# Kernel tuning notes

Hardware: AMD Instinct MI355X
Metric: run time of the kernel (lower is better)

The kernel has to match this reference:

```python
import jax, jax.numpy as jnp
import numpy as np

L, D, H, B, SX, SY, VS, VT = 6, 1024, 16, 4, 512, 512, 32000, 32000
DK = D // H
FF = 4 * D
EPS = 1e-3          # LayerNorm eps (added to std, not var)
SCALE_EMB = float(np.sqrt(D))
NEG = -1e30         # stands in for -inf; fully-masked rows are zeroed after softmax


def pos_encoding(length, d):
    # tensor2tensor-style sinusoid: [sin | cos] concatenated along channels
    nt = d // 2
    lti = np.log(1e4) / (nt - 1)
    inv = np.exp(np.arange(nt) * -lti)
    st = np.arange(length)[:, None] * inv[None, :]
    return jnp.asarray(np.concatenate([np.sin(st), np.cos(st)], axis=1), jnp.float32)


def layer_norm(z, a, b):
    # faithful to the torch module: uses unbiased std (ddof=1) and divides by (std + eps)
    mu = z.mean(-1, keepdims=True)
    sig = jnp.sqrt(((z - mu) ** 2).sum(-1, keepdims=True) / (z.shape[-1] - 1))
    return (z - mu) / (sig + EPS) * a + b


def mha(xq, xkv, wq, wk, wv, wo, mask):
    # xq: (b, lq, D), xkv: (b, lk, D); head-chunking of channel dim == reshape to (H, DK)
    b, lq, _ = xq.shape
    q = (xq @ wq.T).reshape(b, lq, H, DK)
    k = (xkv @ wk.T).reshape(b, -1, H, DK)
    v = (xkv @ wv.T).reshape(b, -1, H, DK)
    s = jnp.einsum('bqhd,bkhd->bhqk', q, k) * (1.0 / np.sqrt(DK))
    m = mask[:, None, :, :]
    s = jnp.where(m, s, NEG)
    att = jax.nn.softmax(s, axis=-1)
    att = att * m.any(-1, keepdims=True)  # replicates NaN->0 for fully masked rows
    c = jnp.einsum('bhqk,bkhd->bqhd', att, v).reshape(b, lq, D)
    return c @ wo.T


def setup_inputs():
    key = jax.random.key(0)
    ks = jax.random.split(key, 10)
    s = 0.02
    emb_x = (jax.random.normal(ks[0], (VS, D), jnp.float32) * s).at[0].set(0.0)  # padding_idx=0
    emb_y = (jax.random.normal(ks[1], (VT, D), jnp.float32) * s).at[0].set(0.0)
    return {
        'emb_x': emb_x, 'emb_y': emb_y,
        'enc_qkvo': jax.random.normal(ks[2], (L, 4, D, D), jnp.float32) * s,
        'enc_ln_s': jnp.ones((L, 2, D), jnp.float32), 'enc_ln_b': jnp.zeros((L, 2, D), jnp.float32),
        'enc_w1': jax.random.normal(ks[3], (L, FF, D), jnp.float32) * s, 'enc_b1': jnp.zeros((L, FF), jnp.float32),
        'enc_w2': jax.random.normal(ks[4], (L, D, FF), jnp.float32) * s, 'enc_b2': jnp.zeros((L, D), jnp.float32),
        'dec_qkvo': jax.random.normal(ks[5], (L, 8, D, D), jnp.float32) * s,
        'dec_ln_s': jnp.ones((L, 3, D), jnp.float32), 'dec_ln_b': jnp.zeros((L, 3, D), jnp.float32),
        'dec_w1': jax.random.normal(ks[6], (L, FF, D), jnp.float32) * s, 'dec_b1': jnp.zeros((L, FF), jnp.float32),
        'dec_w2': jax.random.normal(ks[7], (L, D, FF), jnp.float32) * s, 'dec_b2': jnp.zeros((L, D), jnp.float32),
        'x_block': jax.random.randint(ks[8], (B, SX), 0, VS),
        'y_block': jax.random.randint(ks[9], (B, SY), 0, VT),
    }


def reference(emb_x, emb_y, enc_qkvo, enc_ln_s, enc_ln_b, enc_w1, enc_b1, enc_w2, enc_b2,
              dec_qkvo, dec_ln_s, dec_ln_b, dec_w1, dec_b1, dec_w2, dec_b2, x_block, y_block):
    # internal layout (b, len, D); torch code uses (b, D, len) -- math is identical
    ex = emb_x[x_block] * SCALE_EMB + pos_encoding(SX, D)[None]
    ey = emb_y[y_block] * SCALE_EMB + pos_encoding(SY, D)[None]
    xv = x_block != 0
    yv = y_block != 0
    xx = xv[:, :, None] & xv[:, None, :]                                   # (B, qx, kx)
    xy = yv[:, :, None] & xv[:, None, :]                                   # (B, qy, kx)
    yy = (yv[:, :, None] & yv[:, None, :]) & jnp.tril(jnp.ones((SY, SY), bool))[None]
    e = ex
    for i in range(L):
        sub = mha(e, e, enc_qkvo[i, 0], enc_qkvo[i, 1], enc_qkvo[i, 2], enc_qkvo[i, 3], xx)
        e = layer_norm(e + sub, enc_ln_s[i, 0], enc_ln_b[i, 0])
        sub = jax.nn.relu(e @ enc_w1[i].T + enc_b1[i]) @ enc_w2[i].T + enc_b2[i]
        e = layer_norm(e + sub, enc_ln_s[i, 1], enc_ln_b[i, 1])
    z = e
    e = ey
    for i in range(L):
        sub = mha(e, e, dec_qkvo[i, 0], dec_qkvo[i, 1], dec_qkvo[i, 2], dec_qkvo[i, 3], yy)
        e = layer_norm(e + sub, dec_ln_s[i, 0], dec_ln_b[i, 0])
        sub = mha(e, z, dec_qkvo[i, 4], dec_qkvo[i, 5], dec_qkvo[i, 6], dec_qkvo[i, 7], xy)
        e = layer_norm(e + sub, dec_ln_s[i, 1], dec_ln_b[i, 1])
        sub = jax.nn.relu(e @ dec_w1[i].T + dec_b1[i]) @ dec_w2[i].T + dec_b2[i]
        e = layer_norm(e + sub, dec_ln_s[i, 2], dec_ln_b[i, 2])
    return e @ emb_y.T  # tied output projection -> (B, SY, VT)
```

## Files before the change

kernel.cpp:

```cpp
#include <hip/hip_runtime.h>

typedef unsigned short u16;
typedef float f32x4 __attribute__((ext_vector_type(4)));
typedef __bf16 bf16x8 __attribute__((ext_vector_type(8)));
typedef u16 u16x8 __attribute__((ext_vector_type(8)));

#define DEV __device__ __forceinline__

DEV u16 f2bf(float f) {
  unsigned u = __builtin_bit_cast(unsigned, f);
  u += 0x7fffu + ((u >> 16) & 1u);
  return (u16)(u >> 16);
}
DEV float bf2f(u16 b) { return __builtin_bit_cast(float, (unsigned)b << 16); }

DEV float wsum(float v) {
#pragma unroll
  for (int o = 32; o > 0; o >>= 1) v += __shfl_xor(v, o, 64);
  return v;
}
DEV float gmax16(float v) {
#pragma unroll
  for (int o = 8; o > 0; o >>= 1) v = fmaxf(v, __shfl_xor(v, o, 64));
  return v;
}
DEV float gsum16(float v) {
#pragma unroll
  for (int o = 8; o > 0; o >>= 1) v += __shfl_xor(v, o, 64);
  return v;
}

DEV void gld16(const void* g, void* l) {
  __builtin_amdgcn_global_load_lds((const __attribute__((address_space(1))) void*)g,
                                   (__attribute__((address_space(3))) void*)l, 16, 0, 0);
}

template <int N>
DEV void vwait() {
  if constexpr (N == 0) asm volatile("s_waitcnt vmcnt(0)" ::: "memory");
  else if constexpr (N == 2) asm volatile("s_waitcnt vmcnt(2)" ::: "memory");
  else if constexpr (N == 4) asm volatile("s_waitcnt vmcnt(4)" ::: "memory");
  else asm volatile("s_waitcnt vmcnt(6)" ::: "memory");
}

DEV void remap_bxy(int& bx, int& by) {
  const int gx = gridDim.x, gy = gridDim.y;
  const int flat = blockIdx.y * gx + blockIdx.x;
  const int nwg = gx * gy;
  const int q = nwg >> 3, r = nwg & 7;
  const int xcd = flat & 7, li = flat >> 3;
  const int wg = (xcd < r ? xcd * (q + 1) : r * (q + 1) + (xcd - r) * q) + li;
  by = wg % gy;
  bx = wg / gy;
}

template <int BM, int BN, int MODE, int W, int BK>
__global__ __launch_bounds__(256, W) void gemm_k(
    const u16* __restrict__ A, const u16* __restrict__ B, int lda, int ldb, int K,
    const float* __restrict__ bias, const u16* __restrict__ residb,
    int ldc, u16* __restrict__ Cb, u16* __restrict__ qp,
    u16* __restrict__ kp, u16* __restrict__ vp, int n_off) {
  constexpr int FM = BM / 32, FN = BN / 32;
  constexpr int CHA = BM / 8, CHT = (BM + BN) / 8;
  constexpr int KCH = BK / 64;
  __shared__ u16 lds[2][(BM + BN) * BK];
  const int lane = threadIdx.x & 63, wid = threadIdx.x >> 6;
  const int wr = wid >> 1, wc = wid & 1;
  int bx, by;
  remap_bxy(bx, by);
  const u16* gA = A + (long)(by * BM) * lda;
  const u16* gB = B + (long)(bx * BN) * ldb;

  const f32x4 zero4 = {0.f, 0.f, 0.f, 0.f};
  f32x4 acc[FM][FN];
#pragma unroll
  for (int m = 0; m < FM; ++m)
#pragma unroll
    for (int n = 0; n < FN; ++n) acc[m][n] = zero4;

  const int r8 = lane >> 3, sl = lane & 7;

  auto stage = [&](int buf, int kt) {
#pragma unroll
    for (int sub = 0; sub < KCH; ++sub) {
      const int kb = kt * BK + (sub << 6);
      u16* lbase = &lds[buf][sub * (BM + BN) * 64];
#pragma unroll
      for (int c0 = 0; c0 < CHT; c0 += 4) {
        const int c = c0 + wid;
        u16* l = lbase + (c << 9);
        const u16* g;
        if (c < CHA) {
          int r = (c << 3) + r8;
          g = gA + (long)r * lda + kb + ((sl ^ (r & 7)) << 3);
        } else {
          int r = ((c - CHA) << 3) + r8;
          g = gB + (long)r * ldb + kb + ((sl ^ (r & 7)) << 3);
        }
        gld16(g, l);
      }
    }
  };

  const int KT = K / BK;
  stage(0, 0);
  __syncthreads();
  int cur = 0;
  for (int kt = 0; kt < KT; ++kt) {
    if (kt + 1 < KT) stage(cur ^ 1, kt + 1);
#pragma unroll
    for (int q = 0; q < 2 * KCH; ++q) {
      const int kh = q >> 1, kl = q & 1;
      const u16* lA = &lds[cur][kh * (BM + BN) * 64];
      const u16* lB = lA + (BM << 6);
      bf16x8 af[FM], bv[FN];
#pragma unroll
      for (int m = 0; m < FM; ++m) {
        int r = wr * (BM / 2) + m * 16 + (lane & 15);
        int slot = ((kl << 2) | (lane >> 4)) ^ (r & 7);
        af[m] = *(const bf16x8*)(lA + (r << 6) + (slot << 3));
      }
#pragma unroll
      for (int n = 0; n < FN; ++n) {
        int r = wc * (BN / 2) + n * 16 + (lane & 15);
        int slot = ((kl << 2) | (lane >> 4)) ^ (r & 7);
        bv[n] = *(const bf16x8*)(lB + (r << 6) + (slot << 3));
      }
#pragma unroll
      for (int m = 0; m < FM; ++m)
#pragma unroll
        for (int n = 0; n < FN; ++n)
          acc[m][n] = __builtin_amdgcn_mfma_f32_16x16x32_bf16(af[m], bv[n], acc[m][n], 0, 0, 0);
    }
    __syncthreads();
    cur ^= 1;
  }

  const int rb = by * BM + wr * (BM / 2) + ((lane >> 4) << 2);
  const int cb = bx * BN + wc * (BN / 2) + (lane & 15);
  if constexpr (MODE == 2) {
    const bool isV = (bx * BN + n_off) >= 2048;
    if (isV) {
      __syncthreads();
      u16* T = (u16*)&lds[0][0];
      constexpr int TS = BM + 8;
#pragma unroll
      for (int m = 0; m < FM; ++m)
#pragma unroll
        for (int n = 0; n < FN; ++n) {
          int cl = wc * (BN / 2) + n * 16 + (lane & 15);
#pragma unroll
          for (int j = 0; j < 4; ++j) {
            int rl = wr * (BM / 2) + m * 16 + ((lane >> 4) << 2) + j;
            T[cl * TS + rl] = f2bf(acc[m][n][j]);
          }
        }
      __syncthreads();
      const int vcb = bx * BN + n_off - 2048;
      const int b = (by * BM) >> 9, s0 = (by * BM) & 511;
#pragma unroll
      for (int p = 0; p < BM * BN / 2048; ++p) {
        int idx = p * 2048 + threadIdx.x * 8;
        int dl = idx / BM, slx = idx & (BM - 1);
        u16x8 o;
#pragma unroll
        for (int e = 0; e < 8; ++e) o[e] = T[dl * TS + slx + e];
        int vc = vcb + dl;
        *(u16x8*)(vp + (((long)b * 16 + (vc >> 6)) * 64 + (vc & 63)) * 512 + s0 + slx) = o;
      }
    } else {
#pragma unroll
      for (int m = 0; m < FM; ++m)
#pragma unroll
        for (int n = 0; n < FN; ++n)
#pragma unroll
          for (int j = 0; j < 4; ++j) {
            const int row = rb + m * 16 + j;
            const int np = cb + n * 16 + n_off;
            const int sel = np >> 10, dim = np & 1023;
            long base = (((long)(row >> 9) * 16 + (dim >> 6)) * 512 + (row & 511)) * 64 + (dim & 63);
            u16 val = f2bf(acc[m][n][j]);
            if (sel == 0) qp[base] = val;
            else kp[base] = val;
          }
    }
  } else {
#pragma unroll
    for (int m = 0; m < FM; ++m)
#pragma unroll
      for (int n = 0; n < FN; ++n)
#pragma unroll
        for (int j = 0; j < 4; ++j) {
          const int row = rb + m * 16 + j;
          const int col = cb + n * 16;
          float v = acc[m][n][j];
          if constexpr (MODE == 0) {
            if (bias) v += bias[col];
            if (residb) v += bf2f(residb[(long)row * ldc + col]);
            Cb[(long)row * ldc + col] = f2bf(v);
          } else {
            Cb[(long)row * ldc + col] = f2bf(fmaxf(v + bias[col], 0.f));
          }
        }
  }
}

__global__ __launch_bounds__(512, 1) void gemm256_k(
    const u16* __restrict__ A, const u16* __restrict__ B, int lda, int ldb, int K,
    float* __restrict__ Cf, int ldc) {
  __shared__ u16 As[2][256 * 64];
  __shared__ u16 Bs[2][256 * 64];
  const int lane = threadIdx.x & 63, wid = threadIdx.x >> 6;
  const int wr = wid >> 2, wc = wid & 3;
  int bx, by;
  remap_bxy(bx, by);
  const u16* gA = A + (long)(by * 256) * lda;
  const u16* gB = B + (long)(bx * 256) * ldb;

  const f32x4 z4 = {0.f, 0.f, 0.f, 0.f};
  f32x4 acc[8][4];
#pragma unroll
  for (int m = 0; m < 8; ++m)
#pragma unroll
    for (int n = 0; n < 4; ++n) acc[m][n] = z4;

  const int ssl = lane & 7;

  auto stageH = [&](int t, int h) {
    const int kb = t << 6;
    const int buf = t & 1;
    const bool isA = (h == 0) || (h == 3);
    u16* ldsb = isA ? &As[buf][0] : &Bs[buf][0];
    const u16* gsrc = isA ? gA : gB;
    const int ld = isA ? lda : ldb;
    const int rbase = (h >= 2) ? 128 : 0;
#pragma unroll
    for (int rr = 0; rr < 2; ++rr) {
      const int r0 = rbase + rr * 64 + (wid << 3);
      const int r = r0 + (lane >> 3);
      gld16(gsrc + (long)r * ld + kb + ((ssl ^ (r & 7)) << 3), ldsb + (r0 << 6));
    }
  };

  const int KT = K >> 6;
  stageH(0, 0);
  stageH(0, 1);
  stageH(0, 2);
  stageH(0, 3);

  for (int t = 0; t < KT; ++t) {
    const int buf = t & 1;
    const bool more = (t + 1 < KT);
    const u16* lA = &As[buf][0];
    const u16* lB = &Bs[buf][0];
    bf16x8 af[4][2], bvl[2][2], bvh[2][2];

    vwait<4>();
    __builtin_amdgcn_s_barrier();
    __builtin_amdgcn_sched_barrier(0);
#pragma unroll
    for (int m = 0; m < 4; ++m)
#pragma unroll
      for (int kk = 0; kk < 2; ++kk) {
        int r = wr * 64 + m * 16 + (lane & 15);
        int sg = ((kk << 2) | (lane >> 4)) ^ (r & 7);
        af[m][kk] = *(const bf16x8*)(lA + (r << 6) + (sg << 3));
      }
#pragma unroll
    for (int n = 0; n < 2; ++n)
#pragma unroll
      for (int kk = 0; kk < 2; ++kk) {
        int c = wc * 32 + n * 16 + (lane & 15);
        int sg = ((kk << 2) | (lane >> 4)) ^ (c & 7);
        bvl[n][kk] = *(const bf16x8*)(lB + (c << 6) + (sg << 3));
      }
    if (more) stageH(t + 1, 0);
    __builtin_amdgcn_s_setprio(1);
#pragma unroll
    for (int kk = 0; kk < 2; ++kk)
#pragma unroll
      for (int m = 0; m < 4; ++m)
#pragma unroll
        for (int n = 0; n < 2; ++n)
          acc[m][n] = __builtin_amdgcn_mfma_f32_16x16x32_bf16(af[m][kk], bvl[n][kk], acc[m][n], 0, 0, 0);
    __builtin_amdgcn_s_setprio(0);

    if (more) vwait<4>();
    else vwait<2>();
    __builtin_amdgcn_s_barrier();
    __builtin_amdgcn_sched_barrier(0);
#pragma unroll
    for (int n = 0; n < 2; ++n)
#pragma unroll
      for (int kk = 0; kk < 2; ++kk) {
        int c = 128 + wc * 32 + n * 16 + (lane & 15);
        int sg = ((kk << 2) | (lane >> 4)) ^ (c & 7);
        bvh[n][kk] = *(const bf16x8*)(lB + (c << 6) + (sg << 3));
      }
    if (more) stageH(t + 1, 1);
    __builtin_amdgcn_s_setprio(1);
#pragma unroll
    for (int kk = 0; kk < 2; ++kk)
#pragma unroll
      for (int m = 0; m < 4; ++m)
#pragma unroll
        for (int n = 0; n < 2; ++n)
          acc[m][2 + n] = __builtin_amdgcn_mfma_f32_16x16x32_bf16(af[m][kk], bvh[n][kk], acc[m][2 + n], 0, 0, 0);
    __builtin_amdgcn_s_setprio(0);

    if (more) vwait<4>();
    else vwait<0>();
    __builtin_amdgcn_s_barrier();
    __builtin_amdgcn_sched_barrier(0);
#pragma unroll
    for (int m = 0; m < 4; ++m)
#pragma unroll
      for (int kk = 0; kk < 2; ++kk) {
        int r = 128 + wr * 64 + m * 16 + (lane & 15);
        int sg = ((kk << 2) | (lane >> 4)) ^ (r & 7);
        af[m][kk] = *(const bf16x8*)(lA + (r << 6) + (sg << 3));
      }
    if (more) stageH(t + 1, 2);
    __builtin_amdgcn_s_setprio(1);
#pragma unroll
    for (int kk = 0; kk < 2; ++kk)
#pragma unroll
      for (int m = 0; m < 4; ++m)
#pragma unroll
        for (int n = 0; n < 2; ++n)
          acc[4 + m][2 + n] = __builtin_amdgcn_mfma_f32_16x16x32_bf16(af[m][kk], bvh[n][kk], acc[4 + m][2 + n], 0, 0, 0);
    __builtin_amdgcn_s_setprio(0);

    __builtin_amdgcn_s_barrier();
    __builtin_amdgcn_sched_barrier(0);
    if (more) stageH(t + 1, 3);
    __builtin_amdgcn_s_setprio(1);
#pragma unroll
    for (int kk = 0; kk < 2; ++kk)
#pragma unroll
      for (int m = 0; m < 4; ++m)
#pragma unroll
        for (int n = 0; n < 2; ++n)
          acc[4 + m][n] = __builtin_amdgcn_mfma_f32_16x16x32_bf16(af[m][kk], bvl[n][kk], acc[4 + m][n], 0, 0, 0);
    __builtin_amdgcn_s_setprio(0);
  }

  const int rb = by * 256 + wr * 64 + ((lane >> 4) << 2);
  const int cb = bx * 256 + wc * 32 + (lane & 15);
#pragma unroll
  for (int mi = 0; mi < 8; ++mi)
#pragma unroll
    for (int ni = 0; ni < 4; ++ni)
#pragma unroll
      for (int j = 0; j < 4; ++j) {
        int row = rb + (mi & 3) * 16 + ((mi >> 2) << 7) + j;
        int col = cb + (ni & 1) * 16 + ((ni >> 1) << 7);
        Cf[(long)row * ldc + col] = acc[mi][ni][j];
      }
}

template <int CAUSAL>
__global__ __launch_bounds__(512, 2) void fattn_k(
    const u16* __restrict__ Qg, const u16* __restrict__ Kg, const u16* __restrict__ Vtg,
    const int* __restrict__ qids, const int* __restrict__ kids, u16* __restrict__ ctx) {
  __shared__ u16 Qs[128 * 64];
  __shared__ u16 Ks[3][64 * 64];
  __shared__ u16 Vs[3][64 * 64];
  __shared__ u16 Ps[8][16 * 64];
  const int lane = threadIdx.x & 63, wid = threadIdx.x >> 6;
  const int qt = blockIdx.x, bh = blockIdx.y, b = bh >> 4, h = bh & 15;
  const int q0 = qt << 7;
  const u16* Qbase = Qg + ((long)bh * 512 + q0) * 64;
  const u16* Kbase = Kg + (long)bh * 512 * 64;
  const u16* Vbase = Vtg + (long)bh * 64 * 512;
  const int r8 = lane >> 3, sl = lane & 7;

#pragma unroll
  for (int c0 = 0; c0 < 16; c0 += 8) {
    int c = c0 + wid;
    int r = (c << 3) + r8;
    gld16(Qbase + (long)r * 64 + ((sl ^ (r & 7)) << 3), &Qs[c << 9]);
  }

  auto stageKV = [&](int buf, int kt) {
#pragma unroll
    for (int c0 = 0; c0 < 16; c0 += 8) {
      int c = c0 + wid;
      if (c < 8) {
        int r = (c << 3) + r8;
        gld16(Kbase + (long)(kt * 64 + r) * 64 + ((sl ^ (r & 7)) << 3), &Ks[buf][c << 9]);
      } else {
        int r = ((c - 8) << 3) + r8;
        gld16(Vbase + (long)r * 512 + kt * 64 + ((sl ^ (r & 7)) << 3), &Vs[buf][(c - 8) << 9]);
      }
    }
  };

  const int NKT = CAUSAL ? ((q0 >> 6) + 2) : 8;
  stageKV(0, 0);
  if (NKT > 1) stageKV(1, 1);
  if (NKT > 1) vwait<2>();
  else vwait<0>();
  __builtin_amdgcn_s_barrier();

  const f32x4 z4 = {0.f, 0.f, 0.f, 0.f};
  f32x4 oacc[4];
  float mrun[4], lrun[4];
  bool qv[4];
#pragma unroll
  for (int j = 0; j < 4; ++j) {
    mrun[j] = -3e38f;
    lrun[j] = 0.f;
    int qg = q0 + wid * 16 + ((lane >> 4) << 2) + j;
    qv[j] = qids[(b << 9) + qg] != 0;
  }
#pragma unroll
  for (int nd = 0; nd < 4; ++nd) oacc[nd] = z4;

  for (int kt = 0; kt < NKT; ++kt) {
    const int cur = kt % 3;
    if (kt + 2 < NKT) stageKV((kt + 2) % 3, kt + 2);
    f32x4 s[4];
#pragma unroll
    for (int n = 0; n < 4; ++n) s[n] = z4;
    __builtin_amdgcn_s_setprio(1);
#pragma unroll
    for (int kk = 0; kk < 2; ++kk) {
      bf16x8 aq, bk[4];
      int r = wid * 16 + (lane & 15);
      int slot = ((kk << 2) | (lane >> 4)) ^ (r & 7);
      aq = *(const bf16x8*)&Qs[(r << 6) + (slot << 3)];
#pragma unroll
      for (int n = 0; n < 4; ++n) {
        int c = n * 16 + (lane & 15);
        int slt = ((kk << 2) | (lane >> 4)) ^ (c & 7);
        bk[n] = *(const bf16x8*)&Ks[cur][(c << 6) + (slt << 3)];
      }
#pragma unroll
      for (int n = 0; n < 4; ++n)
        s[n] = __builtin_amdgcn_mfma_f32_16x16x32_bf16(aq, bk[n], s[n], 0, 0, 0);
    }
    __builtin_amdgcn_s_setprio(0);
    bool kvld[4];
#pragma unroll
    for (int n = 0; n < 4; ++n)
      kvld[n] = kids[(b << 9) + (kt << 6) + (n << 4) + (lane & 15)] != 0;
    float mx[4];
#pragma unroll
    for (int j = 0; j < 4; ++j) {
      mx[j] = -3e38f;
      int qg = q0 + wid * 16 + ((lane >> 4) << 2) + j;
#pragma unroll
      for (int n = 0; n < 4; ++n) {
        int colg = (kt << 6) + (n << 4) + (lane & 15);
        bool ok = qv[j] && kvld[n] && (!CAUSAL || colg <= qg);
        float sv = ok ? s[n][j] * 0.125f : -3e38f;
        s[n][j] = sv;
        mx[j] = fmaxf(mx[j], sv);
      }
      mx[j] = gmax16(mx[j]);
    }
#pragma unroll
    for (int j = 0; j < 4; ++j) {
      float mn = fmaxf(mrun[j], mx[j]);
      float f = __expf(mrun[j] - mn);
      mrun[j] = mn;
      float ps = 0.f;
#pragma unroll
      for (int n = 0; n < 4; ++n) {
        float sv = s[n][j];
        float p = (sv > -1e37f) ? __expf(sv - mn) : 0.f;
        s[n][j] = p;
        ps += p;
      }
      ps = gsum16(ps);
      lrun[j] = lrun[j] * f + ps;
#pragma unroll
      for (int nd = 0; nd < 4; ++nd) oacc[nd][j] *= f;
    }
#pragma unroll
    for (int n = 0; n < 4; ++n)
#pragma unroll
      for (int j = 0; j < 4; ++j) {
        int rl = ((lane >> 4) << 2) + j;
        int slot = ((n << 1) | ((lane >> 3) & 1)) ^ (rl & 7);
        Ps[wid][(rl << 6) + (slot << 3) + (lane & 7)] = f2bf(s[n][j]);
      }
    __builtin_amdgcn_s_setprio(1);
#pragma unroll
    for (int kk = 0; kk < 2; ++kk) {
      bf16x8 pa, vv[4];
      int r = lane & 15;
      int slot = ((kk << 2) | (lane >> 4)) ^ (r & 7);
      pa = *(const bf16x8*)&Ps[wid][(r << 6) + (slot << 3)];
#pragma unroll
      for (int nd = 0; nd < 4; ++nd) {
        int rv = (nd << 4) + (lane & 15);
        int slt = ((kk << 2) | (lane >> 4)) ^ (rv & 7);
        vv[nd] = *(const bf16x8*)&Vs[cur][(rv << 6) + (slt << 3)];
      }
#pragma unroll
      for (int nd = 0; nd < 4; ++nd)
        oacc[nd] = __builtin_amdgcn_mfma_f32_16x16x32_bf16(pa, vv[nd], oacc[nd], 0, 0, 0);
    }
    __builtin_amdgcn_s_setprio(0);
    const int ahead = NKT - 1 - kt;
    if (ahead >= 2) {
      vwait<2>();
      __builtin_amdgcn_s_barrier();
    } else if (ahead == 1) {
      vwait<0>();
      __builtin_amdgcn_s_barrier();
    }
  }
#pragma unroll
  for (int j = 0; j < 4; ++j) {
    float inv = (lrun[j] > 0.f) ? 1.0f / lrun[j] : 0.f;
    int qg = q0 + wid * 16 + ((lane >> 4) << 2) + j;
    long rowb = (((long)(b << 9) + qg) * 16 + h) * 64;
#pragma unroll
    for (int nd = 0; nd < 4; ++nd) {
      int d = (nd << 4) + (lane & 15);
      ctx[rowb + d] = f2bf(oacc[nd][j] * inv);
    }
  }
}

__global__ __launch_bounds__(256) void embed_k(const int* __restrict__ ids,
                                               const float* __restrict__ emb,
                                               u16* __restrict__ bfo) {
  const int tok = blockIdx.x, t = threadIdx.x;
  const int s = tok & 511;
  const long id = ids[tok];
  const int d = t * 4;
  float4 ev = *(const float4*)(emb + id * 1024 + d);
  float o[4] = {ev.x * 32.f, ev.y * 32.f, ev.z * 32.f, ev.w * 32.f};
#pragma unroll
  for (int j = 0; j < 4; ++j) {
    int dd = d + j, di = dd & 511;
    float ang = (float)s * expf(-(float)di * 0.0180241494559220821f);
    o[j] += (dd < 512) ? sinf(ang) : cosf(ang);
  }
  ushort4 ob = {f2bf(o[0]), f2bf(o[1]), f2bf(o[2]), f2bf(o[3])};
  *(ushort4*)(bfo + (long)tok * 1024 + d) = ob;
}

__global__ __launch_bounds__(256) void ln_k(const u16* __restrict__ vin,
                                            const float* __restrict__ gam,
                                            const float* __restrict__ bet,
                                            u16* __restrict__ bfo) {
  __shared__ float red[8];
  const int row = blockIdx.x, t = threadIdx.x;
  const ushort4 xv = *(const ushort4*)(vin + (long)row * 1024 + t * 4);
  float v0 = bf2f(xv.x), v1 = bf2f(xv.y), v2 = bf2f(xv.z), v3 = bf2f(xv.w);
  float sm = wsum(v0 + v1 + v2 + v3);
  if ((t & 63) == 0) red[t >> 6] = sm;
  __syncthreads();
  const float mu = (red[0] + red[1] + red[2] + red[3]) * (1.0f / 1024.0f);
  const float d0 = v0 - mu, d1 = v1 - mu, d2 = v2 - mu, d3 = v3 - mu;
  float ss = wsum(d0 * d0 + d1 * d1 + d2 * d2 + d3 * d3);
  if ((t & 63) == 0) red[4 + (t >> 6)] = ss;
  __syncthreads();
  const float sig = sqrtf((red[4] + red[5] + red[6] + red[7]) * (1.0f / 1023.0f));
  const float inv = 1.0f / (sig + 0.001f);
  const float4 g4 = *(const float4*)(gam + t * 4);
  const float4 b4 = *(const float4*)(bet + t * 4);
  const float o0 = d0 * inv * g4.x + b4.x, o1 = d1 * inv * g4.y + b4.y;
  const float o2 = d2 * inv * g4.z + b4.z, o3 = d3 * inv * g4.w + b4.w;
  ushort4 ob = {f2bf(o0), f2bf(o1), f2bf(o2), f2bf(o3)};
  *(ushort4*)(bfo + (long)row * 1024 + t * 4) = ob;
}

__global__ void cvt_k(const float* __restrict__ src, u16* __restrict__ dst, int n4) {
  for (int i = blockIdx.x * 256 + threadIdx.x; i < n4; i += gridDim.x * 256) {
    float4 v = ((const float4*)src)[i];
    ushort4 o = {f2bf(v.x), f2bf(v.y), f2bf(v.z), f2bf(v.w)};
    ((ushort4*)dst)[i] = o;
  }
}

__global__ void cvt3_k(const float* __restrict__ s0, int n0, const float* __restrict__ s1,
                       int n1, const float* __restrict__ s2, int n2, u16* __restrict__ dst) {
  const int tot = n0 + n1 + n2;
  for (int i = blockIdx.x * 256 + threadIdx.x; i < tot; i += gridDim.x * 256) {
    const float* s;
    int j;
    if (i < n0) { s = s0; j = i; }
    else if (i < n0 + n1) { s = s1; j = i - n0; }
    else { s = s2; j = i - n0 - n1; }
    float4 v = ((const float4*)s)[j];
    ushort4 o = {f2bf(v.x), f2bf(v.y), f2bf(v.z), f2bf(v.w)};
    ((ushort4*)dst)[i] = o;
  }
}

extern "C" void kernel_launch(void* const* d_in, const int* in_sizes, int n_in, void* d_out,
                              int out_size, void* d_ws, size_t ws_size, hipStream_t stream) {
  (void)in_sizes; (void)n_in; (void)out_size;
  const float* emb_x = (const float*)d_in[0];
  const float* emb_y = (const float*)d_in[1];
  const float* enc_qkvo = (const float*)d_in[2];
  const float* enc_ln_s = (const float*)d_in[3];
  const float* enc_ln_b = (const float*)d_in[4];
  const float* enc_w1 = (const float*)d_in[5];
  const float* enc_b1 = (const float*)d_in[6];
  const float* enc_w2 = (const float*)d_in[7];
  const float* enc_b2 = (const float*)d_in[8];
  const float* dec_qkvo = (const float*)d_in[9];
  const float* dec_ln_s = (const float*)d_in[10];
  const float* dec_ln_b = (const float*)d_in[11];
  const float* dec_w1 = (const float*)d_in[12];
  const float* dec_b1 = (const float*)d_in[13];
  const float* dec_w2 = (const float*)d_in[14];
  const float* dec_b2 = (const float*)d_in[15];
  const int* x_block = (const int*)d_in[16];
  const int* y_block = (const int*)d_in[17];

  const long TOK = 2048, Dm = 1024, M1 = 1048576;
  char* p = (char*)d_ws;
  auto alloc = [&](long bytes) { char* r = p; p += (bytes + 255) & ~255L; return r; };
  u16* subb = (u16*)alloc(TOK * Dm * 2);
  u16* ebf = (u16*)alloc(TOK * Dm * 2);
  u16* zbf = (u16*)alloc(TOK * Dm * 2);
  u16* qb = (u16*)alloc(TOK * Dm * 2);
  u16* kb = (u16*)alloc(TOK * Dm * 2);
  u16* vtb = (u16*)alloc(TOK * Dm * 2);
  u16* ctx = (u16*)alloc(TOK * Dm * 2);
  u16* hbuf = (u16*)alloc(TOK * 4096 * 2);
  u16* wbuf = (u16*)alloc(16L * M1 * 2);
  u16* embyb = (u16*)alloc(32000L * 1024 * 2);
  if ((size_t)(p - (char*)d_ws) > ws_size) return;

  auto gemmF = [&](const u16* A, const u16* Bw, int M, int N, int K, int lda, int ldb,
                   const float* bias, const u16* residb, u16* C, int ldc) {
    dim3 g(N / 64, M / 64);
    gemm_k<64, 64, 0, 2, 128><<<g, 256, 0, stream>>>(A, Bw, lda, ldb, K, bias, residb,
                                                     ldc, C, nullptr, nullptr, nullptr, 0);
  };
  auto gemmRelu = [&](const u16* A, const u16* Bw, const float* bias, u16* C) {
    dim3 g(32, 16);
    gemm_k<128, 128, 1, 2, 64><<<g, 256, 0, stream>>>(A, Bw, 1024, 1024, 1024, bias, nullptr,
                                                      4096, C, nullptr, nullptr, nullptr, 0);
  };
  auto gemmQKV = [&](const u16* A, const u16* Bw, int N, int n_off) {
    if (N >= 2048) {
      dim3 g(N / 128, 32);
      gemm_k<64, 128, 2, 3, 64><<<g, 256, 0, stream>>>(A, Bw, 1024, 1024, 1024, nullptr,
                                                       nullptr, 0, nullptr, qb, kb, vtb,
                                                       n_off);
    } else {
      dim3 g(N / 64, 32);
      gemm_k<64, 64, 2, 4, 64><<<g, 256, 0, stream>>>(A, Bw, 1024, 1024, 1024, nullptr,
                                                      nullptr, 0, nullptr, qb, kb, vtb,
                                                      n_off);
    }
  };
  auto attn = [&](const int* qids, const int* kids, int causal) {
    if (causal)
      fattn_k<1><<<dim3(4, 64), 512, 0, stream>>>(qb, kb, vtb, qids, kids, ctx);
    else
      fattn_k<0><<<dim3(4, 64), 512, 0, stream>>>(qb, kb, vtb, qids, kids, ctx);
  };
  auto lnorm = [&](const float* g, const float* b) {
    ln_k<<<2048, 256, 0, stream>>>(subb, g, b, ebf);
  };

  cvt_k<<<2048, 256, 0, stream>>>(emb_y, embyb, 32000 * 1024 / 4);

  embed_k<<<2048, 256, 0, stream>>>(x_block, emb_x, ebf);
  for (int i = 0; i < 6; ++i) {
    cvt3_k<<<2048, 256, 0, stream>>>(enc_qkvo + (long)i * 4 * M1, (int)M1,
                                     enc_w1 + (long)i * 4 * M1, (int)M1,
                                     enc_w2 + (long)i * 4 * M1, (int)M1, wbuf);
    gemmQKV(ebf, wbuf, 3072, 0);
    attn(x_block, x_block, 0);
    gemmF(ctx, wbuf + 3L * M1, 2048, 1024, 1024, 1024, 1024, nullptr, ebf, subb, 1024);
    lnorm(enc_ln_s + (i * 2 + 0) * 1024, enc_ln_b + (i * 2 + 0) * 1024);
    gemmRelu(ebf, wbuf + 4L * M1, enc_b1 + i * 4096, hbuf);
    gemmF(hbuf, wbuf + 8L * M1, 2048, 1024, 4096, 4096, 4096, enc_b2 + i * 1024, ebf,
          subb, 1024);
    lnorm(enc_ln_s + (i * 2 + 1) * 1024, enc_ln_b + (i * 2 + 1) * 1024);
  }
  hipMemcpyAsync(zbf, ebf, TOK * Dm * 2, hipMemcpyDeviceToDevice, stream);

  embed_k<<<2048, 256, 0, stream>>>(y_block, emb_y, ebf);
  for (int i = 0; i < 6; ++i) {
    cvt3_k<<<2048, 256, 0, stream>>>(dec_qkvo + (long)i * 8 * M1, (int)(2 * M1),
                                     dec_w1 + (long)i * 4 * M1, (int)M1,
                                     dec_w2 + (long)i * 4 * M1, (int)M1, wbuf);
    gemmQKV(ebf, wbuf, 3072, 0);
    attn(y_block, y_block, 1);
    gemmF(ctx, wbuf + 3L * M1, 2048, 1024, 1024, 1024, 1024, nullptr, ebf, subb, 1024);
    lnorm(dec_ln_s + (i * 3 + 0) * 1024, dec_ln_b + (i * 3 + 0) * 1024);
    gemmQKV(ebf, wbuf + 4L * M1, 1024, 0);
    gemmQKV(zbf, wbuf + 5L * M1, 2048, 1024);
    attn(y_block, x_block, 0);
    gemmF(ctx, wbuf + 7L * M1, 2048, 1024, 1024, 1024, 1024, nullptr, ebf, subb, 1024);
    lnorm(dec_ln_s + (i * 3 + 1) * 1024, dec_ln_b + (i * 3 + 1) * 1024);
    gemmRelu(ebf, wbuf + 8L * M1, dec_b1 + i * 4096, hbuf);
    gemmF(hbuf, wbuf + 12L * M1, 2048, 1024, 4096, 4096, 4096, dec_b2 + i * 1024, ebf,
          subb, 1024);
    lnorm(dec_ln_s + (i * 3 + 2) * 1024, dec_ln_b + (i * 3 + 2) * 1024);
  }
  gemm256_k<<<dim3(125, 8), 512, 0, stream>>>(ebf, embyb, 1024, 1024, 1024,
                                              (float*)d_out, 32000);
}
```

Measured before the change: 2.210 ms.

## Batch weight conversion into one launch per stack and fuse cross-attention Q/KV GEMMs

When the workspace is large enough, all encoder weights and then all decoder weights are converted to bf16 in a single large cvt3 launch each, replacing twelve small per-layer conversion kernels. The decoder's separate Q GEMM (on the decoder state) and KV GEMM (on encoder output) are merged into one launch using a new mode that picks the A matrix per column block. This cuts launch count and gives the GEMMs bigger grids, at the cost of needing a much larger workspace and adding a fallback path.

```diff
diff --git a/kernel.cpp b/kernel.cpp
--- a/kernel.cpp
+++ b/kernel.cpp
@@ -56,7 +56,8 @@
 
 template <int BM, int BN, int MODE, int W, int BK>
 __global__ __launch_bounds__(256, W) void gemm_k(
-    const u16* __restrict__ A, const u16* __restrict__ B, int lda, int ldb, int K,
+    const u16* __restrict__ A, const u16* __restrict__ A2,
+    const u16* __restrict__ B, int lda, int ldb, int K,
     const float* __restrict__ bias, const u16* __restrict__ residb,
     int ldc, u16* __restrict__ Cb, u16* __restrict__ qp,
     u16* __restrict__ kp, u16* __restrict__ vp, int n_off) {
@@ -68,7 +69,11 @@
   const int wr = wid >> 1, wc = wid & 1;
   int bx, by;
   remap_bxy(bx, by);
-  const u16* gA = A + (long)(by * BM) * lda;
+  const u16* Abase = A;
+  if constexpr (MODE == 3) {
+    if (bx * BN >= 1024) Abase = A2;
+  }
+  const u16* gA = Abase + (long)(by * BM) * lda;
   const u16* gB = B + (long)(bx * BN) * ldb;
 
   const f32x4 zero4 = {0.f, 0.f, 0.f, 0.f};
@@ -138,7 +143,7 @@
 
   const int rb = by * BM + wr * (BM / 2) + ((lane >> 4) << 2);
   const int cb = bx * BN + wc * (BN / 2) + (lane & 15);
-  if constexpr (MODE == 2) {
+  if constexpr (MODE == 2 || MODE == 3) {
     const bool isV = (bx * BN + n_off) >= 2048;
     if (isV) {
       __syncthreads();
@@ -627,33 +632,36 @@
   u16* vtb = (u16*)alloc(TOK * Dm * 2);
   u16* ctx = (u16*)alloc(TOK * Dm * 2);
   u16* hbuf = (u16*)alloc(TOK * 4096 * 2);
-  u16* wbuf = (u16*)alloc(16L * M1 * 2);
   u16* embyb = (u16*)alloc(32000L * 1024 * 2);
+  size_t used = (size_t)(p - (char*)d_ws);
+  const bool mega = (used + 96L * M1 * 2 + 4096) <= ws_size;
+  u16* wall = (u16*)alloc(mega ? 96L * M1 * 2 : 16L * M1 * 2);
   if ((size_t)(p - (char*)d_ws) > ws_size) return;
 
   auto gemmF = [&](const u16* A, const u16* Bw, int M, int N, int K, int lda, int ldb,
                    const float* bias, const u16* residb, u16* C, int ldc) {
     dim3 g(N / 64, M / 64);
-    gemm_k<64, 64, 0, 2, 128><<<g, 256, 0, stream>>>(A, Bw, lda, ldb, K, bias, residb,
-                                                     ldc, C, nullptr, nullptr, nullptr, 0);
+    gemm_k<64, 64, 0, 2, 128><<<g, 256, 0, stream>>>(A, nullptr, Bw, lda, ldb, K, bias,
+                                                     residb, ldc, C, nullptr, nullptr,
+                                                     nullptr, 0);
   };
   auto gemmRelu = [&](const u16* A, const u16* Bw, const float* bias, u16* C) {
     dim3 g(32, 16);
-    gemm_k<128, 128, 1, 2, 64><<<g, 256, 0, stream>>>(A, Bw, 1024, 1024, 1024, bias, nullptr,
-                                                      4096, C, nullptr, nullptr, nullptr, 0);
-  };
-  auto gemmQKV = [&](const u16* A, const u16* Bw, int N, int n_off) {
-    if (N >= 2048) {
-      dim3 g(N / 128, 32);
-      gemm_k<64, 128, 2, 3, 64><<<g, 256, 0, stream>>>(A, Bw, 1024, 1024, 1024, nullptr,
-                                                       nullptr, 0, nullptr, qb, kb, vtb,
-                                                       n_off);
-    } else {
-      dim3 g(N / 64, 32);
-      gemm_k<64, 64, 2, 4, 64><<<g, 256, 0, stream>>>(A, Bw, 1024, 1024, 1024, nullptr,
-                                                      nullptr, 0, nullptr, qb, kb, vtb,
-                                                      n_off);
-    }
+    gemm_k<128, 128, 1, 2, 64><<<g, 256, 0, stream>>>(A, nullptr, Bw, 1024, 1024, 1024, bias,
+                                                      nullptr, 4096, C, nullptr, nullptr,
+                                                      nullptr, 0);
+  };
+  auto gemmQKV = [&](const u16* A, const u16* Bw) {
+    dim3 g(24, 32);
+    gemm_k<64, 128, 2, 3, 64><<<g, 256, 0, stream>>>(A, nullptr, Bw, 1024, 1024, 1024,
+                                                     nullptr, nullptr, 0, nullptr, qb, kb,
+                                                     vtb, 0);
+  };
+  auto gemmQKVx = [&](const u16* Aq, const u16* Akv, const u16* Bw) {
+    dim3 g(24, 32);
+    gemm_k<64, 128, 3, 3, 64><<<g, 256, 0, stream>>>(Aq, Akv, Bw, 1024, 1024, 1024,
+                                                     nullptr, nullptr, 0, nullptr, qb, kb,
+                                                     vtb, 0);
   };
   auto attn = [&](const int* qids, const int* kids, int causal) {
     if (causal)
@@ -668,38 +676,63 @@
   cvt_k<<<2048, 256, 0, stream>>>(emb_y, embyb, 32000 * 1024 / 4);
 
   embed_k<<<2048, 256, 0, stream>>>(x_block, emb_x, ebf);
+  if (mega) {
+    cvt3_k<<<2048, 256, 0, stream>>>(enc_qkvo, (int)(6 * M1), enc_w1, (int)(6 * M1),
+                                     enc_w2, (int)(6 * M1), wall);
+  }
   for (int i = 0; i < 6; ++i) {
-    cvt3_k<<<2048, 256, 0, stream>>>(enc_qkvo + (long)i * 4 * M1, (int)M1,
-                                     enc_w1 + (long)i * 4 * M1, (int)M1,
-                                     enc_w2 + (long)i * 4 * M1, (int)M1, wbuf);
-    gemmQKV(ebf, wbuf, 3072, 0);
+    u16 *Wqkvo, *Ww1, *Ww2;
+    if (mega) {
+      Wqkvo = wall + (long)i * 4 * M1;
+      Ww1 = wall + 24L * M1 + (long)i * 4 * M1;
+      Ww2 = wall + 48L * M1 + (long)i * 4 * M1;
+    } else {
+      cvt3_k<<<2048, 256, 0, stream>>>(enc_qkvo + (long)i * 4 * M1, (int)M1,
+                                       enc_w1 + (long)i * 4 * M1, (int)M1,
+                                       enc_w2 + (long)i * 4 * M1, (int)M1, wall);
+      Wqkvo = wall;
+      Ww1 = wall + 4L * M1;
+      Ww2 = wall + 8L * M1;
+    }
+    gemmQKV(ebf, Wqkvo);
     attn(x_block, x_block, 0);
-    gemmF(ctx, wbuf + 3L * M1, 2048, 1024, 1024, 1024, 1024, nullptr, ebf, subb, 1024);
+    gemmF(ctx, Wqkvo + 3L * M1, 2048, 1024, 1024, 1024, 1024, nullptr, ebf, subb, 1024);
     lnorm(enc_ln_s + (i * 2 + 0) * 1024, enc_ln_b + (i * 2 + 0) * 1024);
-    gemmRelu(ebf, wbuf + 4L * M1, enc_b1 + i * 4096, hbuf);
-    gemmF(hbuf, wbuf + 8L * M1, 2048, 1024, 4096, 4096, 4096, enc_b2 + i * 1024, ebf,
-          subb, 1024);
+    gemmRelu(ebf, Ww1, enc_b1 + i * 4096, hbuf);
+    gemmF(hbuf, Ww2, 2048, 1024, 4096, 4096, 4096, enc_b2 + i * 1024, ebf, subb, 1024);
     lnorm(enc_ln_s + (i * 2 + 1) * 1024, enc_ln_b + (i * 2 + 1) * 1024);
   }
   hipMemcpyAsync(zbf, ebf, TOK * Dm * 2, hipMemcpyDeviceToDevice, stream);
 
   embed_k<<<2048, 256, 0, stream>>>(y_block, emb_y, ebf);
+  if (mega) {
+    cvt3_k<<<2048, 256, 0, stream>>>(dec_qkvo, (int)(12 * M1), dec_w1, (int)(6 * M1),
+                                     dec_w2, (int)(6 * M1), wall);
+  }
   for (int i = 0; i < 6; ++i) {
-    cvt3_k<<<2048, 256, 0, stream>>>(dec_qkvo + (long)i * 8 * M1, (int)(2 * M1),
-                                     dec_w1 + (long)i * 4 * M1, (int)M1,
-                                     dec_w2 + (long)i * 4 * M1, (int)M1, wbuf);
-    gemmQKV(ebf, wbuf, 3072, 0);
+    u16 *Wqkvo, *Ww1, *Ww2;
+    if (mega) {
+      Wqkvo = wall + (long)i * 8 * M1;
+      Ww1 = wall + 48L * M1 + (long)i * 4 * M1;
+      Ww2 = wall + 72L * M1 + (long)i * 4 * M1;
+    } else {
+      cvt3_k<<<2048, 256, 0, stream>>>(dec_qkvo + (long)i * 8 * M1, (int)(2 * M1),
+                                       dec_w1 + (long)i * 4 * M1, (int)M1,
+                                       dec_w2 + (long)i * 4 * M1, (int)M1, wall);
+      Wqkvo = wall;
+      Ww1 = wall + 8L * M1;
+      Ww2 = wall + 12L * M1;
+    }
+    gemmQKV(ebf, Wqkvo);
     attn(y_block, y_block, 1);
-    gemmF(ctx, wbuf + 3L * M1, 2048, 1024, 1024, 1024, 1024, nullptr, ebf, subb, 1024);
+    gemmF(ctx, Wqkvo + 3L * M1, 2048, 1024, 1024, 1024, 1024, nullptr, ebf, subb, 1024);
     lnorm(dec_ln_s + (i * 3 + 0) * 1024, dec_ln_b + (i * 3 + 0) * 1024);
-    gemmQKV(ebf, wbuf + 4L * M1, 1024, 0);
-    gemmQKV(zbf, wbuf + 5L * M1, 2048, 1024);
+    gemmQKVx(ebf, zbf, Wqkvo + 4L * M1);
     attn(y_block, x_block, 0);
-    gemmF(ctx, wbuf + 7L * M1, 2048, 1024, 1024, 1024, 1024, nullptr, ebf, subb, 1024);
+    gemmF(ctx, Wqkvo + 7L * M1, 2048, 1024, 1024, 1024, 1024, nullptr, ebf, subb, 1024);
     lnorm(dec_ln_s + (i * 3 + 1) * 1024, dec_ln_b + (i * 3 + 1) * 1024);
-    gemmRelu(ebf, wbuf + 8L * M1, dec_b1 + i * 4096, hbuf);
-    gemmF(hbuf, wbuf + 12L * M1, 2048, 1024, 4096, 4096, 4096, dec_b2 + i * 1024, ebf,
-          subb, 1024);
+    gemmRelu(ebf, Ww1, dec_b1 + i * 4096, hbuf);
+    gemmF(hbuf, Ww2, 2048, 1024, 4096, 4096, 4096, dec_b2 + i * 1024, ebf, subb, 1024);
     lnorm(dec_ln_s + (i * 3 + 2) * 1024, dec_ln_b + (i * 3 + 2) * 1024);
   }
   gemm256_k<<<dim3(125, 8), 512, 0, stream>>>(ebf, embyb, 1024, 1024, 1024,
```

Result: slower. 2.364 ms (+7.0%).
